# Kernel tuning notes

Hardware: AMD Instinct MI355X
Metric: run time of the kernel (lower is better)

## Reference

```python
import jax, jax.numpy as jnp
import numpy as np

HIDDEN = 1024
N_HEADS = 16
HEAD_DIM = HIDDEN // N_HEADS


def setup_inputs() -> dict:
    key = jax.random.key(0)
    ks = jax.random.split(key, 7)
    b, l, m = 4, 1024, 1024
    q = jax.random.normal(ks[0], (b, l, HIDDEN), dtype=jnp.float32)
    k = jax.random.normal(ks[1], (b, m, HIDDEN), dtype=jnp.float32)
    v = jax.random.normal(ks[2], (b, m, HIDDEN), dtype=jnp.float32)
    s = 1.0 / np.sqrt(HIDDEN)
    w_q = jax.random.normal(ks[3], (HIDDEN, HIDDEN), dtype=jnp.float32) * s
    w_k = jax.random.normal(ks[4], (HIDDEN, HIDDEN), dtype=jnp.float32) * s
    w_v = jax.random.normal(ks[5], (HIDDEN, HIDDEN), dtype=jnp.float32) * s
    w_o = jax.random.normal(ks[6], (HIDDEN, HIDDEN), dtype=jnp.float32) * s
    return {"q": q, "k": k, "v": v, "w_q": w_q, "w_k": w_k, "w_v": w_v, "w_o": w_o}


def reference(q, k, v, w_q, w_k, w_v, w_o):
    b, l, _ = q.shape
    _, m, _ = k.shape
    # Linear (bias=False): y = x @ W^T
    qp = q @ w_q.T
    kp = k @ w_k.T
    vp = v @ w_v.T  # projected but unused downstream (faithful to original bug)
    # Faithful non-standard split: hidden -> (head_dim, n_heads)
    qh = qp.reshape(b, l, HEAD_DIM, N_HEADS)
    kh = kp.reshape(b, m, HEAD_DIM, N_HEADS)
    # attn over K, scaled, softmax over m (dim=2)
    scores = jnp.einsum('bldn,bmdn->blmn', qh, kh) / np.sqrt(HEAD_DIM)
    attn = jax.nn.softmax(scores, axis=2)
    # dropout is identity in eval mode
    # NOTE: original attends over K (not V) — reproduced faithfully
    x = jnp.einsum('blmn,bmdn->bldn', attn, kh)
    x = x.reshape(b, l, HIDDEN)  # 'b l d n -> b l (d n)'
    return x @ w_o.T
```

## Files before the change

### kernel.cpp

```cpp
#include <hip/hip_runtime.h>
#include <hip/hip_bf16.h>
#include <stdint.h>
#include <math.h>


typedef __bf16 bf16;
typedef __bf16 bf16x8 __attribute__((ext_vector_type(8)));
typedef __bf16 bf16x4 __attribute__((ext_vector_type(4)));
typedef float  f32x4  __attribute__((ext_vector_type(4)));

__device__ __forceinline__ void async_load16(const void* g, void* l) {
  __builtin_amdgcn_global_load_lds((__attribute__((address_space(1))) void*)g,
                                   (__attribute__((address_space(3))) void*)l,
                                   16, 0, 0);
}

__device__ __forceinline__ void join_pin() {
  __builtin_amdgcn_sched_barrier(0);
  __builtin_amdgcn_s_barrier();
  __builtin_amdgcn_sched_barrier(0);
}

__device__ __forceinline__ int detect_fl(const void* samp, int tid, int* smax) {
  int e = (((const unsigned short*)samp)[tid] >> 7) & 0xFF;
#pragma unroll
  for (int off = 1; off <= 32; off <<= 1) {
    int o = __shfl_xor(e, off);
    e = o > e ? o : e;
  }
  if ((tid & 63) == 0) smax[tid >> 6] = e;
  __syncthreads();
  int m01 = smax[0] > smax[1] ? smax[0] : smax[1];
  int m23 = smax[2] > smax[3] ? smax[2] : smax[3];
  return ((m01 > m23 ? m01 : m23) >= 140) ? 1 : 0;
}

__global__ void __launch_bounds__(256)
canon(const void* __restrict__ q, const void* __restrict__ k,
      const void* __restrict__ wq, const void* __restrict__ wk,
      const void* __restrict__ wo,
      bf16* __restrict__ qc, bf16* __restrict__ kc,
      bf16* __restrict__ wqc, bf16* __restrict__ wkc,
      bf16* __restrict__ wo_p, int* __restrict__ flag) {
  __shared__ int smax[4];
  const int tid = threadIdx.x;
  const int fl = detect_fl(q, tid, smax);
  if (blockIdx.x == 0 && tid == 0) *flag = fl;

  const size_t e0 = (size_t)blockIdx.x * 2048 + tid * 8;
  const size_t M4 = 4194304, M8 = 8388608, M9 = 9437184, M10 = 10485760;
  const void* src; bf16* dst; size_t le; bool perm = false;
  if (e0 < M4)       { src = q;  dst = qc;   le = e0;       }
  else if (e0 < M8)  { src = k;  dst = kc;   le = e0 - M4;  }
  else if (e0 < M9)  { src = wq; dst = wqc;  le = e0 - M8;  }
  else if (e0 < M10) { src = wk; dst = wkc;  le = e0 - M9;  }
  else               { src = wo; dst = wo_p; le = e0 - M10; perm = true; }

  if (!perm) {
    bf16x8 v;
    if (fl) {
      const float* p = (const float*)src + le;
      f32x4 a = *(const f32x4*)p, b = *(const f32x4*)(p + 4);
#pragma unroll
      for (int j = 0; j < 4; ++j) { v[j] = (bf16)a[j]; v[4 + j] = (bf16)b[j]; }
    } else {
      v = *(const bf16x8*)((const bf16*)src + le);
    }
    *(bf16x8*)(dst + le) = v;
  } else {
    int o = (int)(le >> 10), kp0 = (int)(le & 1023);
    bf16x8 v;
#pragma unroll
    for (int j = 0; j < 8; ++j) {
      int kp = kp0 + j;
      int h = ((kp & 63) << 4) | (kp >> 6);
      float f = fl ? ((const float*)src)[o * 1024 + h]
                   : (float)((const bf16*)src)[o * 1024 + h];
      f = fminf(fmaxf(f, -1024.f), 1024.f);
      v[j] = (bf16)f;
    }
    *(bf16x8*)(dst + le) = v;
  }
}

__global__ void __launch_bounds__(256, 3)
qk_gemm(const bf16* __restrict__ qc, const bf16* __restrict__ wqc,
        const bf16* __restrict__ kc, const bf16* __restrict__ wkc,
        bf16* __restrict__ qh, bf16* __restrict__ kh, bf16* __restrict__ khT,
        float cs) {
  __shared__ __align__(16) char smem[49152];
  bf16* const sA0 = (bf16*)smem;
  bf16* const sA1 = (bf16*)(smem + 16384);
  bf16* const sB0 = (bf16*)(smem + 32768);
  bf16* const sB1 = (bf16*)(smem + 40960);
  bf16* const epi = (bf16*)smem;

  const int tid  = threadIdx.x;
  const int lane = tid & 63;
  const int wave = tid >> 6;
  const int q4   = lane >> 4;
  const int c16  = lane & 15;
  const int wm   = wave >> 1;
  const int wn   = wave & 1;

  const int z = blockIdx.z;
  const bf16* A = z ? kc : qc;
  const bf16* W = z ? wkc : wqc;
  const float scale = z ? 1.0f : cs;
  bf16* out0 = z ? kh : qh;

  const int lin    = blockIdx.x + 8 * blockIdx.y;
  const int rowBlk = (lin & 31) * 128;
  const int colBlk = (lin >> 5) * 64;

  const bf16* gA[4]; int lA[4];
#pragma unroll
  for (int i = 0; i < 4; ++i) {
    int s = tid + 256 * i;
    int r = s >> 3, g = (s & 7) ^ (r & 7);
    gA[i] = A + (size_t)(rowBlk + r) * 1024 + g * 8;
    lA[i] = s * 8;
  }
  const bf16* gB[2]; int lB[2];
#pragma unroll
  for (int i = 0; i < 2; ++i) {
    int s = tid + 256 * i;
    int r = s >> 3, g = (s & 7) ^ (r & 7);
    gB[i] = W + (size_t)(colBlk + r) * 1024 + g * 8;
    lB[i] = s * 8;
  }

  f32x4 acc[4][2] = {};

#pragma unroll
  for (int i = 0; i < 4; ++i) async_load16(gA[i], sA0 + lA[i]);
#pragma unroll
  for (int i = 0; i < 2; ++i) async_load16(gB[i], sB0 + lB[i]);

  for (int t = 0; t < 16; ++t) {
    if (t < 15) {
      const int kn = (t + 1) * 64;
      bf16* dA = (t & 1) ? sA0 : sA1;
      bf16* dB = (t & 1) ? sB0 : sB1;
#pragma unroll
      for (int i = 0; i < 4; ++i) async_load16(gA[i] + kn, dA + lA[i]);
#pragma unroll
      for (int i = 0; i < 2; ++i) async_load16(gB[i] + kn, dB + lB[i]);
      asm volatile("s_waitcnt vmcnt(6)" ::: "memory");
    } else {
      asm volatile("s_waitcnt vmcnt(0)" ::: "memory");
    }
    join_pin();

    const bf16* cA = (t & 1) ? sA1 : sA0;
    const bf16* cB = (t & 1) ? sB1 : sB0;
#pragma unroll
    for (int ks = 0; ks < 2; ++ks) {
      bf16x8 af[4], bfr[2];
#pragma unroll
      for (int mt = 0; mt < 4; ++mt) {
        int row = wm * 64 + mt * 16 + c16;
        af[mt] = *(const bf16x8*)(cA + row * 64 +
                   (((ks * 4 + q4) ^ (row & 7)) * 8));
      }
#pragma unroll
      for (int nt = 0; nt < 2; ++nt) {
        int row = wn * 32 + nt * 16 + c16;
        bfr[nt] = *(const bf16x8*)(cB + row * 64 +
                   (((ks * 4 + q4) ^ (row & 7)) * 8));
      }
#pragma unroll
      for (int mt = 0; mt < 4; ++mt)
#pragma unroll
        for (int nt = 0; nt < 2; ++nt)
          acc[mt][nt] = __builtin_amdgcn_mfma_f32_16x16x32_bf16(
              af[mt], bfr[nt], acc[mt][nt], 0, 0, 0);
    }
    asm volatile("s_waitcnt lgkmcnt(0)" ::: "memory");
    join_pin();
  }

#pragma unroll
  for (int mt = 0; mt < 4; ++mt)
#pragma unroll
    for (int nt = 0; nt < 2; ++nt)
#pragma unroll
      for (int r = 0; r < 4; ++r) {
        int m_t = wm * 64 + mt * 16 + q4 * 4 + r;
        int c   = wn * 32 + nt * 16 + c16;
        epi[m_t * 70 + c] = (bf16)(acc[mt][nt][r] * scale);
      }
  __syncthreads();

  const int bb    = rowBlk >> 10;
  const int mbase = rowBlk & 1023;
  const int dg0   = colBlk >> 4;

  {
    int n = tid >> 4;
#pragma unroll
    for (int i = 0; i < 8; ++i) {
      int m_t = (tid & 15) + i * 16;
      bf16x4 v;
#pragma unroll
      for (int dt = 0; dt < 4; ++dt) v[dt] = epi[m_t * 70 + dt * 16 + n];
      *(bf16x4*)(out0 + ((size_t)(bb * 16 + n) * 1024 + mbase + m_t) * 64 + dg0) = v;
    }
  }
  if (z) {
    int r = tid >> 2, qtr = tid & 3;
    int n = r >> 2, dt = r & 3;
    int c = dt * 16 + n;
    size_t base = ((size_t)(bb * 16 + n) * 64 + dg0 + dt) * 1024 + mbase + qtr * 32;
#pragma unroll
    for (int c8 = 0; c8 < 4; ++c8) {
      bf16x8 v;
#pragma unroll
      for (int j = 0; j < 8; ++j) v[j] = epi[(qtr * 32 + c8 * 8 + j) * 70 + c];
      *(bf16x8*)(khT + base + c8 * 8) = v;
    }
  }
}

__global__ void __launch_bounds__(256, 3)
attn_kernel(const bf16* __restrict__ qh, const bf16* __restrict__ kh,
            const bf16* __restrict__ khT, bf16* __restrict__ xh) {
  __shared__ __align__(16) bf16 sK[2][64 * 64];
  __shared__ __align__(16) bf16 sKT[2][64 * 64];
  __shared__ __align__(16) bf16 sP[4][16 * 72];

  const int tid  = threadIdx.x;
  const int lane = tid & 63;
  const int wave = tid >> 6;
  const int q4   = lane >> 4;
  const int c16  = lane & 15;
  const int lin  = blockIdx.x;
  const int bn   = lin & 63;
  const int qt   = lin >> 6;
  const int b    = bn >> 4, n = bn & 15;
  const int l0w  = qt * 64 + wave * 16;

  const bf16* qhead  = qh  + (size_t)bn * (1024 * 64);
  const bf16* khead  = kh  + (size_t)bn * (1024 * 64);
  const bf16* kThead = khT + (size_t)bn * (64 * 1024);

  bf16x8 aq[2];
#pragma unroll
  for (int hh = 0; hh < 2; ++hh)
    aq[hh] = *(const bf16x8*)(qhead + (size_t)(l0w + c16) * 64 + hh * 32 + q4 * 8);

  int kr[2], kg[2];
#pragma unroll
  for (int i = 0; i < 2; ++i) {
    int s = tid + 256 * i;
    kr[i] = s >> 3;  kg[i] = (s & 7) ^ (kr[i] & 7);
  }

  f32x4 O[4] = {};
  f32x4 Osum = {};
  bf16x8 ones;
#pragma unroll
  for (int j = 0; j < 8; ++j) ones[j] = (bf16)1.0f;
  bf16* sPw = sP[wave];

#pragma unroll
  for (int i = 0; i < 2; ++i) {
    int s = (tid + 256 * i) * 8;
    async_load16(khead + (size_t)kr[i] * 64 + kg[i] * 8, &sK[0][s]);
    async_load16(kThead + (size_t)kr[i] * 1024 + kg[i] * 8, &sKT[0][s]);
  }

  for (int t = 0; t < 16; ++t) {
    if (t < 15) {
      const int m0n = (t + 1) * 64;
      const int bi  = (t + 1) & 1;
#pragma unroll
      for (int i = 0; i < 2; ++i) {
        int s = (tid + 256 * i) * 8;
        async_load16(khead + (size_t)(m0n + kr[i]) * 64 + kg[i] * 8, &sK[bi][s]);
        async_load16(kThead + (size_t)kr[i] * 1024 + m0n + kg[i] * 8, &sKT[bi][s]);
      }
      asm volatile("s_waitcnt vmcnt(4)" ::: "memory");
    } else {
      asm volatile("s_waitcnt vmcnt(0)" ::: "memory");
    }
    join_pin();

    const bf16* cK  = sK[t & 1];
    const bf16* cKT = sKT[t & 1];

    f32x4 S[4] = {};
    __builtin_amdgcn_s_setprio(1);
#pragma unroll
    for (int t4 = 0; t4 < 4; ++t4) {
#pragma unroll
      for (int hh = 0; hh < 2; ++hh) {
        int row = t4 * 16 + c16;
        bf16x8 bk = *(const bf16x8*)(cK + row * 64 +
                                     (((hh * 4 + q4) ^ (row & 7)) * 8));
        S[t4] = __builtin_amdgcn_mfma_f32_16x16x32_bf16(aq[hh], bk, S[t4], 0, 0, 0);
      }
    }
    __builtin_amdgcn_s_setprio(0);

#pragma unroll
    for (int t4 = 0; t4 < 4; ++t4)
#pragma unroll
      for (int r = 0; r < 4; ++r) {
        float p = __builtin_amdgcn_exp2f(S[t4][r]);
        sPw[(q4 * 4 + r) * 72 + t4 * 16 + c16] = (bf16)p;
      }

    bf16x8 ap[2];
    __builtin_amdgcn_s_setprio(1);
#pragma unroll
    for (int kk2 = 0; kk2 < 2; ++kk2) {
      ap[kk2] = *(const bf16x8*)(sPw + c16 * 72 + kk2 * 32 + q4 * 8);
      Osum = __builtin_amdgcn_mfma_f32_16x16x32_bf16(ap[kk2], ones, Osum, 0, 0, 0);
    }

#pragma unroll
    for (int td = 0; td < 4; ++td) {
#pragma unroll
      for (int kk2 = 0; kk2 < 2; ++kk2) {
        int row = td * 16 + c16;
        bf16x8 bkt = *(const bf16x8*)(cKT + row * 64 +
                                      (((kk2 * 4 + q4) ^ (row & 7)) * 8));
        O[td] = __builtin_amdgcn_mfma_f32_16x16x32_bf16(ap[kk2], bkt, O[td], 0, 0, 0);
      }
    }
    __builtin_amdgcn_s_setprio(0);
    asm volatile("s_waitcnt lgkmcnt(0)" ::: "memory");
    join_pin();
  }

  {
    float inv[4];
#pragma unroll
    for (int r = 0; r < 4; ++r) inv[r] = 1.0f / Osum[r];
#pragma unroll
    for (int td = 0; td < 4; ++td)
#pragma unroll
      for (int r = 0; r < 4; ++r)
        sPw[(q4 * 4 + r) * 72 + td * 16 + c16] = (bf16)(O[td][r] * inv[r]);
  }
  {
    int l_loc = lane >> 2, dq = lane & 3;
    bf16x8 v0 = *(const bf16x8*)(sPw + l_loc * 72 + dq * 16);
    bf16x8 v1 = *(const bf16x8*)(sPw + l_loc * 72 + dq * 16 + 8);
    size_t base = ((size_t)(b * 1024 + l0w + l_loc) * 16 + n) * 64 + dq * 16;
    *(bf16x8*)(xh + base)     = v0;
    *(bf16x8*)(xh + base + 8) = v1;
  }
}

__global__ void __launch_bounds__(256, 4)
o_gemm(const bf16* __restrict__ A, const bf16* __restrict__ W,
       bf16* __restrict__ out0, float* __restrict__ outf,
       const int* __restrict__ flag) {
  __shared__ __align__(16) bf16 sA[2][64 * 64];
  __shared__ __align__(16) bf16 sB[2][64 * 64];

  const int tid  = threadIdx.x;
  const int lane = tid & 63;
  const int wave = tid >> 6;
  const int q4   = lane >> 4;
  const int c16  = lane & 15;
  const int wm   = wave >> 1;
  const int wn   = wave & 1;

  const int lin    = blockIdx.x + 8 * blockIdx.y;
  const int rowBlk = (lin & 63) * 64;
  const int colBlk = (lin >> 6) * 64;

  const bf16* gA[2]; const bf16* gB[2]; int ls[2];
#pragma unroll
  for (int i = 0; i < 2; ++i) {
    int s = tid + 256 * i;
    int r = s >> 3, g = (s & 7) ^ (r & 7);
    gA[i] = A + (size_t)(rowBlk + r) * 1024 + g * 8;
    gB[i] = W + (size_t)(colBlk + r) * 1024 + g * 8;
    ls[i] = s * 8;
  }

  f32x4 acc[2][2] = {};

#pragma unroll
  for (int i = 0; i < 2; ++i) {
    async_load16(gA[i], &sA[0][ls[i]]);
    async_load16(gB[i], &sB[0][ls[i]]);
  }

  for (int t = 0; t < 16; ++t) {
    if (t < 15) {
      const int kn = (t + 1) * 64;
      const int bi = (t + 1) & 1;
#pragma unroll
      for (int i = 0; i < 2; ++i) {
        async_load16(gA[i] + kn, &sA[bi][ls[i]]);
        async_load16(gB[i] + kn, &sB[bi][ls[i]]);
      }
      asm volatile("s_waitcnt vmcnt(4)" ::: "memory");
    } else {
      asm volatile("s_waitcnt vmcnt(0)" ::: "memory");
    }
    join_pin();

    const bf16* cA = sA[t & 1];
    const bf16* cB = sB[t & 1];
#pragma unroll
    for (int ks = 0; ks < 2; ++ks) {
      bf16x8 af[2], bfr[2];
#pragma unroll
      for (int mt = 0; mt < 2; ++mt) {
        int row = wm * 32 + mt * 16 + c16;
        af[mt] = *(const bf16x8*)(cA + row * 64 +
                   (((ks * 4 + q4) ^ (row & 7)) * 8));
      }
#pragma unroll
      for (int nt = 0; nt < 2; ++nt) {
        int row = wn * 32 + nt * 16 + c16;
        bfr[nt] = *(const bf16x8*)(cB + row * 64 +
                   (((ks * 4 + q4) ^ (row & 7)) * 8));
      }
#pragma unroll
      for (int mt = 0; mt < 2; ++mt)
#pragma unroll
        for (int nt = 0; nt < 2; ++nt)
          acc[mt][nt] = __builtin_amdgcn_mfma_f32_16x16x32_bf16(
              af[mt], bfr[nt], acc[mt][nt], 0, 0, 0);
    }
    asm volatile("s_waitcnt lgkmcnt(0)" ::: "memory");
    join_pin();
  }

  const int fl = *flag;
#pragma unroll
  for (int mt = 0; mt < 2; ++mt)
#pragma unroll
    for (int nt = 0; nt < 2; ++nt)
#pragma unroll
      for (int r = 0; r < 4; ++r) {
        int gm = rowBlk + wm * 32 + mt * 16 + q4 * 4 + r;
        int gn = colBlk + wn * 32 + nt * 16 + c16;
        size_t idx = (size_t)gm * 1024 + gn;
        if (fl) outf[idx] = acc[mt][nt][r];
        else    out0[idx] = (bf16)acc[mt][nt][r];
      }
}

extern "C" void kernel_launch(void* const* d_in, const int* in_sizes, int n_in,
                              void* d_out, int out_size, void* d_ws, size_t ws_size,
                              hipStream_t stream) {
  const void* q_raw  = d_in[0];
  const void* k_raw  = d_in[1];
  const void* wq_raw = d_in[3];
  const void* wk_raw = d_in[4];
  const void* wo_raw = d_in[6];

  char* ws = (char*)d_ws;
  const size_t MB = 1024 * 1024;
  bf16* qc   = (bf16*)(ws + 0 * MB);
  bf16* kc   = (bf16*)(ws + 8 * MB);
  bf16* kh   = (bf16*)(ws + 16 * MB);
  bf16* wqc  = (bf16*)(ws + 24 * MB);
  bf16* wkc  = (bf16*)(ws + 26 * MB);
  bf16* wo_p = (bf16*)(ws + 28 * MB);
  int*  flag = (int*)(ws + 30 * MB);
  bf16* xh   = qc;
  bf16* qh   = (bf16*)d_out;
  bf16* khT  = (bf16*)((char*)d_out + 8 * MB);

  const float CS = 0.125f * 1.4426950408889634f;
  dim3 blk(256, 1, 1);

  hipLaunchKernelGGL(canon, dim3(5632), blk, 0, stream,
                     q_raw, k_raw, wq_raw, wk_raw, wo_raw,
                     qc, kc, wqc, wkc, wo_p, flag);
  hipLaunchKernelGGL(qk_gemm, dim3(8, 64, 2), blk, 0, stream,
                     qc, wqc, kc, wkc, qh, kh, khT, CS);
  hipLaunchKernelGGL(attn_kernel, dim3(1024), blk, 0, stream,
                     qh, kh, khT, xh);
  hipLaunchKernelGGL(o_gemm, dim3(8, 128), blk, 0, stream,
                     xh, wo_p, (bf16*)d_out, (float*)d_out, flag);
}
```

Measured before the change: 194.3 us.

## Restructure attention into single-wave blocks reading K directly from global memory

```diff
diff --git a/kernel.cpp b/kernel.cpp
--- a/kernel.cpp
+++ b/kernel.cpp
@@ -222,135 +222,110 @@
   }
 }
 
-__global__ void __launch_bounds__(256, 3)
+__global__ void __launch_bounds__(64, 4)
 attn_kernel(const bf16* __restrict__ qh, const bf16* __restrict__ kh,
             const bf16* __restrict__ khT, bf16* __restrict__ xh) {
-  __shared__ __align__(16) bf16 sK[2][64 * 64];
-  __shared__ __align__(16) bf16 sKT[2][64 * 64];
-  __shared__ __align__(16) bf16 sP[4][16 * 72];
-
-  const int tid  = threadIdx.x;
-  const int lane = tid & 63;
-  const int wave = tid >> 6;
+  __shared__ __align__(16) bf16 sPw[32 * 72];
+
+  const int lane = threadIdx.x & 63;
   const int q4   = lane >> 4;
   const int c16  = lane & 15;
   const int lin  = blockIdx.x;
   const int bn   = lin & 63;
   const int qt   = lin >> 6;
   const int b    = bn >> 4, n = bn & 15;
-  const int l0w  = qt * 64 + wave * 16;
+  const int l0w  = qt * 32;
 
   const bf16* qhead  = qh  + (size_t)bn * (1024 * 64);
   const bf16* khead  = kh  + (size_t)bn * (1024 * 64);
   const bf16* kThead = khT + (size_t)bn * (64 * 1024);
 
-  bf16x8 aq[2];
-#pragma unroll
-  for (int hh = 0; hh < 2; ++hh)
-    aq[hh] = *(const bf16x8*)(qhead + (size_t)(l0w + c16) * 64 + hh * 32 + q4 * 8);
-
-  int kr[2], kg[2];
-#pragma unroll
-  for (int i = 0; i < 2; ++i) {
-    int s = tid + 256 * i;
-    kr[i] = s >> 3;  kg[i] = (s & 7) ^ (kr[i] & 7);
-  }
-
-  f32x4 O[4] = {};
-  f32x4 Osum = {};
+  bf16x8 aq[2][2];
+#pragma unroll
+  for (int g = 0; g < 2; ++g)
+#pragma unroll
+    for (int hh = 0; hh < 2; ++hh)
+      aq[g][hh] = *(const bf16x8*)(qhead +
+                    (size_t)(l0w + g * 16 + c16) * 64 + hh * 32 + q4 * 8);
+
+  f32x4 O[2][4] = {};
+  f32x4 Osum[2] = {};
   bf16x8 ones;
 #pragma unroll
   for (int j = 0; j < 8; ++j) ones[j] = (bf16)1.0f;
-  bf16* sPw = sP[wave];
-
-#pragma unroll
-  for (int i = 0; i < 2; ++i) {
-    int s = (tid + 256 * i) * 8;
-    async_load16(khead + (size_t)kr[i] * 64 + kg[i] * 8, &sK[0][s]);
-    async_load16(kThead + (size_t)kr[i] * 1024 + kg[i] * 8, &sKT[0][s]);
-  }
 
   for (int t = 0; t < 16; ++t) {
-    if (t < 15) {
-      const int m0n = (t + 1) * 64;
-      const int bi  = (t + 1) & 1;
-#pragma unroll
-      for (int i = 0; i < 2; ++i) {
-        int s = (tid + 256 * i) * 8;
-        async_load16(khead + (size_t)(m0n + kr[i]) * 64 + kg[i] * 8, &sK[bi][s]);
-        async_load16(kThead + (size_t)kr[i] * 1024 + m0n + kg[i] * 8, &sKT[bi][s]);
-      }
-      asm volatile("s_waitcnt vmcnt(4)" ::: "memory");
-    } else {
-      asm volatile("s_waitcnt vmcnt(0)" ::: "memory");
-    }
-    join_pin();
-
-    const bf16* cK  = sK[t & 1];
-    const bf16* cKT = sKT[t & 1];
-
-    f32x4 S[4] = {};
+    const int m0 = t * 64;
+
+    f32x4 S[2][4] = {};
     __builtin_amdgcn_s_setprio(1);
 #pragma unroll
     for (int t4 = 0; t4 < 4; ++t4) {
 #pragma unroll
       for (int hh = 0; hh < 2; ++hh) {
-        int row = t4 * 16 + c16;
-        bf16x8 bk = *(const bf16x8*)(cK + row * 64 +
-                                     (((hh * 4 + q4) ^ (row & 7)) * 8));
-        S[t4] = __builtin_amdgcn_mfma_f32_16x16x32_bf16(aq[hh], bk, S[t4], 0, 0, 0);
+        bf16x8 bk = *(const bf16x8*)(khead +
+                      (size_t)(m0 + t4 * 16 + c16) * 64 + hh * 32 + q4 * 8);
+        S[0][t4] = __builtin_amdgcn_mfma_f32_16x16x32_bf16(aq[0][hh], bk, S[0][t4], 0, 0, 0);
+        S[1][t4] = __builtin_amdgcn_mfma_f32_16x16x32_bf16(aq[1][hh], bk, S[1][t4], 0, 0, 0);
       }
     }
     __builtin_amdgcn_s_setprio(0);
 
 #pragma unroll
-    for (int t4 = 0; t4 < 4; ++t4)
-#pragma unroll
-      for (int r = 0; r < 4; ++r) {
-        float p = __builtin_amdgcn_exp2f(S[t4][r]);
-        sPw[(q4 * 4 + r) * 72 + t4 * 16 + c16] = (bf16)p;
-      }
-
-    bf16x8 ap[2];
+    for (int g = 0; g < 2; ++g)
+#pragma unroll
+      for (int t4 = 0; t4 < 4; ++t4)
+#pragma unroll
+        for (int r = 0; r < 4; ++r) {
+          float p = __builtin_amdgcn_exp2f(S[g][t4][r]);
+          sPw[(g * 16 + q4 * 4 + r) * 72 + t4 * 16 + c16] = (bf16)p;
+        }
+
+    bf16x8 ap[2][2];
     __builtin_amdgcn_s_setprio(1);
 #pragma unroll
-    for (int kk2 = 0; kk2 < 2; ++kk2) {
-      ap[kk2] = *(const bf16x8*)(sPw + c16 * 72 + kk2 * 32 + q4 * 8);
-      Osum = __builtin_amdgcn_mfma_f32_16x16x32_bf16(ap[kk2], ones, Osum, 0, 0, 0);
-    }
+    for (int g = 0; g < 2; ++g)
+#pragma unroll
+      for (int kk2 = 0; kk2 < 2; ++kk2) {
+        ap[g][kk2] = *(const bf16x8*)(sPw + (g * 16 + c16) * 72 +
+                                      kk2 * 32 + q4 * 8);
+        Osum[g] = __builtin_amdgcn_mfma_f32_16x16x32_bf16(ap[g][kk2], ones, Osum[g], 0, 0, 0);
+      }
 
 #pragma unroll
     for (int td = 0; td < 4; ++td) {
 #pragma unroll
       for (int kk2 = 0; kk2 < 2; ++kk2) {
-        int row = td * 16 + c16;
-        bf16x8 bkt = *(const bf16x8*)(cKT + row * 64 +
-                                      (((kk2 * 4 + q4) ^ (row & 7)) * 8));
-        O[td] = __builtin_amdgcn_mfma_f32_16x16x32_bf16(ap[kk2], bkt, O[td], 0, 0, 0);
+        bf16x8 bkt = *(const bf16x8*)(kThead +
+                       (size_t)(td * 16 + c16) * 1024 + m0 + kk2 * 32 + q4 * 8);
+        O[0][td] = __builtin_amdgcn_mfma_f32_16x16x32_bf16(ap[0][kk2], bkt, O[0][td], 0, 0, 0);
+        O[1][td] = __builtin_amdgcn_mfma_f32_16x16x32_bf16(ap[1][kk2], bkt, O[1][td], 0, 0, 0);
       }
     }
     __builtin_amdgcn_s_setprio(0);
-    asm volatile("s_waitcnt lgkmcnt(0)" ::: "memory");
-    join_pin();
-  }
-
-  {
+  }
+
+#pragma unroll
+  for (int g = 0; g < 2; ++g) {
     float inv[4];
 #pragma unroll
-    for (int r = 0; r < 4; ++r) inv[r] = 1.0f / Osum[r];
+    for (int r = 0; r < 4; ++r) inv[r] = 1.0f / Osum[g][r];
 #pragma unroll
     for (int td = 0; td < 4; ++td)
 #pragma unroll
       for (int r = 0; r < 4; ++r)
-        sPw[(q4 * 4 + r) * 72 + td * 16 + c16] = (bf16)(O[td][r] * inv[r]);
+        sPw[(g * 16 + q4 * 4 + r) * 72 + td * 16 + c16] = (bf16)(O[g][td][r] * inv[r]);
   }
   {
     int l_loc = lane >> 2, dq = lane & 3;
-    bf16x8 v0 = *(const bf16x8*)(sPw + l_loc * 72 + dq * 16);
-    bf16x8 v1 = *(const bf16x8*)(sPw + l_loc * 72 + dq * 16 + 8);
-    size_t base = ((size_t)(b * 1024 + l0w + l_loc) * 16 + n) * 64 + dq * 16;
-    *(bf16x8*)(xh + base)     = v0;
-    *(bf16x8*)(xh + base + 8) = v1;
+#pragma unroll
+    for (int g = 0; g < 2; ++g) {
+      bf16x8 v0 = *(const bf16x8*)(sPw + (g * 16 + l_loc) * 72 + dq * 16);
+      bf16x8 v1 = *(const bf16x8*)(sPw + (g * 16 + l_loc) * 72 + dq * 16 + 8);
+      size_t base = ((size_t)(b * 1024 + l0w + g * 16 + l_loc) * 16 + n) * 64 + dq * 16;
+      *(bf16x8*)(xh + base)     = v0;
+      *(bf16x8*)(xh + base + 8) = v1;
+    }
   }
 }
 
@@ -479,7 +454,7 @@
                      qc, kc, wqc, wkc, wo_p, flag);
   hipLaunchKernelGGL(qk_gemm, dim3(8, 64, 2), blk, 0, stream,
                      qc, wqc, kc, wkc, qh, kh, khT, CS);
-  hipLaunchKernelGGL(attn_kernel, dim3(1024), blk, 0, stream,
+  hipLaunchKernelGGL(attn_kernel, dim3(2048), dim3(64, 1, 1), 0, stream,
                      qh, kh, khT, xh);
   hipLaunchKernelGGL(o_gemm, dim3(8, 128), blk, 0, stream,
                      xh, wo_p, (bf16*)d_out, (float*)d_out, flag);
```

Result: slower. 216.8 us (+11.6%).

## Switch attention kernel to 32x32x16 MFMA with 32-row query tiles per wave

Applied to the files above, without the earlier changes.

```diff
diff --git a/kernel.cpp b/kernel.cpp
--- a/kernel.cpp
+++ b/kernel.cpp
@@ -8,6 +8,7 @@
 typedef __bf16 bf16x8 __attribute__((ext_vector_type(8)));
 typedef __bf16 bf16x4 __attribute__((ext_vector_type(4)));
 typedef float  f32x4  __attribute__((ext_vector_type(4)));
+typedef float  f32x16 __attribute__((ext_vector_type(16)));
 
 __device__ __forceinline__ void async_load16(const void* g, void* l) {
   __builtin_amdgcn_global_load_lds((__attribute__((address_space(1))) void*)g,
@@ -222,32 +223,32 @@
   }
 }
 
-__global__ void __launch_bounds__(256, 3)
+__global__ void __launch_bounds__(256, 2)
 attn_kernel(const bf16* __restrict__ qh, const bf16* __restrict__ kh,
             const bf16* __restrict__ khT, bf16* __restrict__ xh) {
   __shared__ __align__(16) bf16 sK[2][64 * 64];
   __shared__ __align__(16) bf16 sKT[2][64 * 64];
-  __shared__ __align__(16) bf16 sP[4][16 * 72];
+  __shared__ __align__(16) bf16 sP[4][32 * 72];
 
   const int tid  = threadIdx.x;
   const int lane = tid & 63;
   const int wave = tid >> 6;
-  const int q4   = lane >> 4;
-  const int c16  = lane & 15;
+  const int n32  = lane & 31;
+  const int hk   = lane >> 5;
   const int lin  = blockIdx.x;
   const int bn   = lin & 63;
   const int qt   = lin >> 6;
   const int b    = bn >> 4, n = bn & 15;
-  const int l0w  = qt * 64 + wave * 16;
+  const int l0w  = qt * 128 + wave * 32;
 
   const bf16* qhead  = qh  + (size_t)bn * (1024 * 64);
   const bf16* khead  = kh  + (size_t)bn * (1024 * 64);
   const bf16* kThead = khT + (size_t)bn * (64 * 1024);
 
-  bf16x8 aq[2];
-#pragma unroll
-  for (int hh = 0; hh < 2; ++hh)
-    aq[hh] = *(const bf16x8*)(qhead + (size_t)(l0w + c16) * 64 + hh * 32 + q4 * 8);
+  bf16x8 aq[4];
+#pragma unroll
+  for (int kc = 0; kc < 4; ++kc)
+    aq[kc] = *(const bf16x8*)(qhead + (size_t)(l0w + n32) * 64 + kc * 16 + hk * 8);
 
   int kr[2], kg[2];
 #pragma unroll
@@ -256,8 +257,8 @@
     kr[i] = s >> 3;  kg[i] = (s & 7) ^ (kr[i] & 7);
   }
 
-  f32x4 O[4] = {};
-  f32x4 Osum = {};
+  f32x16 O[2] = {};
+  f32x16 Osum = {};
   bf16x8 ones;
 #pragma unroll
   for (int j = 0; j < 8; ++j) ones[j] = (bf16)1.0f;
@@ -289,44 +290,41 @@
     const bf16* cK  = sK[t & 1];
     const bf16* cKT = sKT[t & 1];
 
-    f32x4 S[4] = {};
+    f32x16 S0 = {}, S1 = {};
     __builtin_amdgcn_s_setprio(1);
 #pragma unroll
-    for (int t4 = 0; t4 < 4; ++t4) {
-#pragma unroll
-      for (int hh = 0; hh < 2; ++hh) {
-        int row = t4 * 16 + c16;
-        bf16x8 bk = *(const bf16x8*)(cK + row * 64 +
-                                     (((hh * 4 + q4) ^ (row & 7)) * 8));
-        S[t4] = __builtin_amdgcn_mfma_f32_16x16x32_bf16(aq[hh], bk, S[t4], 0, 0, 0);
-      }
+    for (int kc = 0; kc < 4; ++kc) {
+      int G = kc * 2 + hk;
+      int R0 = n32, R1 = 32 + n32;
+      bf16x8 bk0 = *(const bf16x8*)(cK + R0 * 64 + ((G ^ (R0 & 7)) * 8));
+      bf16x8 bk1 = *(const bf16x8*)(cK + R1 * 64 + ((G ^ (R1 & 7)) * 8));
+      S0 = __builtin_amdgcn_mfma_f32_32x32x16_bf16(aq[kc], bk0, S0, 0, 0, 0);
+      S1 = __builtin_amdgcn_mfma_f32_32x32x16_bf16(aq[kc], bk1, S1, 0, 0, 0);
     }
     __builtin_amdgcn_s_setprio(0);
 
 #pragma unroll
-    for (int t4 = 0; t4 < 4; ++t4)
-#pragma unroll
-      for (int r = 0; r < 4; ++r) {
-        float p = __builtin_amdgcn_exp2f(S[t4][r]);
-        sPw[(q4 * 4 + r) * 72 + t4 * 16 + c16] = (bf16)p;
-      }
-
-    bf16x8 ap[2];
+    for (int r = 0; r < 16; ++r) {
+      int qrow = (r & 3) + 8 * (r >> 2) + 4 * hk;
+      sPw[qrow * 72 + n32]      = (bf16)__builtin_amdgcn_exp2f(S0[r]);
+      sPw[qrow * 72 + 32 + n32] = (bf16)__builtin_amdgcn_exp2f(S1[r]);
+    }
+
+    bf16x8 ap[4];
     __builtin_amdgcn_s_setprio(1);
 #pragma unroll
-    for (int kk2 = 0; kk2 < 2; ++kk2) {
-      ap[kk2] = *(const bf16x8*)(sPw + c16 * 72 + kk2 * 32 + q4 * 8);
-      Osum = __builtin_amdgcn_mfma_f32_16x16x32_bf16(ap[kk2], ones, Osum, 0, 0, 0);
-    }
-
-#pragma unroll
-    for (int td = 0; td < 4; ++td) {
-#pragma unroll
-      for (int kk2 = 0; kk2 < 2; ++kk2) {
-        int row = td * 16 + c16;
-        bf16x8 bkt = *(const bf16x8*)(cKT + row * 64 +
-                                      (((kk2 * 4 + q4) ^ (row & 7)) * 8));
-        O[td] = __builtin_amdgcn_mfma_f32_16x16x32_bf16(ap[kk2], bkt, O[td], 0, 0, 0);
+    for (int kc = 0; kc < 4; ++kc) {
+      ap[kc] = *(const bf16x8*)(sPw + n32 * 72 + kc * 16 + hk * 8);
+      Osum = __builtin_amdgcn_mfma_f32_32x32x16_bf16(ap[kc], ones, Osum, 0, 0, 0);
+    }
+#pragma unroll
+    for (int dt = 0; dt < 2; ++dt) {
+#pragma unroll
+      for (int kc = 0; kc < 4; ++kc) {
+        int R = dt * 32 + n32;
+        int G = kc * 2 + hk;
+        bf16x8 bkt = *(const bf16x8*)(cKT + R * 64 + ((G ^ (R & 7)) * 8));
+        O[dt] = __builtin_amdgcn_mfma_f32_32x32x16_bf16(ap[kc], bkt, O[dt], 0, 0, 0);
       }
     }
     __builtin_amdgcn_s_setprio(0);
@@ -335,22 +333,25 @@
   }
 
   {
-    float inv[4];
-#pragma unroll
-    for (int r = 0; r < 4; ++r) inv[r] = 1.0f / Osum[r];
-#pragma unroll
-    for (int td = 0; td < 4; ++td)
-#pragma unroll
-      for (int r = 0; r < 4; ++r)
-        sPw[(q4 * 4 + r) * 72 + td * 16 + c16] = (bf16)(O[td][r] * inv[r]);
+    float inv[16];
+#pragma unroll
+    for (int r = 0; r < 16; ++r) inv[r] = 1.0f / Osum[r];
+#pragma unroll
+    for (int dt = 0; dt < 2; ++dt)
+#pragma unroll
+      for (int r = 0; r < 16; ++r) {
+        int qrow = (r & 3) + 8 * (r >> 2) + 4 * hk;
+        sPw[qrow * 72 + dt * 32 + n32] = (bf16)(O[dt][r] * inv[r]);
+      }
   }
   {
-    int l_loc = lane >> 2, dq = lane & 3;
-    bf16x8 v0 = *(const bf16x8*)(sPw + l_loc * 72 + dq * 16);
-    bf16x8 v1 = *(const bf16x8*)(sPw + l_loc * 72 + dq * 16 + 8);
-    size_t base = ((size_t)(b * 1024 + l0w + l_loc) * 16 + n) * 64 + dq * 16;
-    *(bf16x8*)(xh + base)     = v0;
-    *(bf16x8*)(xh + base + 8) = v1;
+    int l_loc = lane >> 1, dh = lane & 1;
+    size_t base = ((size_t)(b * 1024 + l0w + l_loc) * 16 + n) * 64 + dh * 32;
+#pragma unroll
+    for (int c8 = 0; c8 < 4; ++c8) {
+      bf16x8 v = *(const bf16x8*)(sPw + l_loc * 72 + dh * 32 + c8 * 8);
+      *(bf16x8*)(xh + base + c8 * 8) = v;
+    }
   }
 }
 
@@ -479,7 +480,7 @@
                      qc, kc, wqc, wkc, wo_p, flag);
   hipLaunchKernelGGL(qk_gemm, dim3(8, 64, 2), blk, 0, stream,
                      qc, wqc, kc, wkc, qh, kh, khT, CS);
-  hipLaunchKernelGGL(attn_kernel, dim3(1024), blk, 0, stream,
+  hipLaunchKernelGGL(attn_kernel, dim3(512), blk, 0, stream,
                      qh, kh, khT, xh);
   hipLaunchKernelGGL(o_gemm, dim3(8, 128), blk, 0, stream,
                      xh, wo_p, (bf16*)d_out, (float*)d_out, flag);
```

Result: faster. 188.3 us (-3.1%).
